# Kernel tuning notes

Hardware: AMD Instinct MI355X
Metric: run time of the kernel (lower is better)

## Reference

```python
import jax, jax.numpy as jnp
import numpy as np

NUM_TAGS = 64
BSZ = 256
SEQ_LEN = 2048


def setup_inputs() -> dict:
    key = jax.random.key(0)
    k1, k2, k3, k4, k5 = jax.random.split(key, 5)
    inputs = jax.random.normal(k1, (BSZ, SEQ_LEN, NUM_TAGS), dtype=jnp.float32)
    tags = jax.random.randint(k2, (BSZ, SEQ_LEN), 0, NUM_TAGS, dtype=jnp.int32)
    mask = jnp.ones((BSZ, SEQ_LEN), dtype=jnp.int32)
    # parameters (xavier-normal-ish transitions, normal start/end)
    std = float(np.sqrt(2.0 / (NUM_TAGS + NUM_TAGS)))
    transitions = jax.random.normal(k3, (NUM_TAGS, NUM_TAGS), dtype=jnp.float32) * std
    start_transitions = jax.random.normal(k4, (NUM_TAGS,), dtype=jnp.float32)
    end_transitions = jax.random.normal(k5, (NUM_TAGS,), dtype=jnp.float32)
    return {"inputs": inputs, "tags": tags, "mask": mask,
            "transitions": transitions,
            "start_transitions": start_transitions,
            "end_transitions": end_transitions}


def _input_likelihood(logits, maskf, transitions, start_transitions, end_transitions):
    # logits: (B, S, T); maskf: (B, S) float
    logits_t = jnp.transpose(logits, (1, 0, 2))   # (S, B, T)
    mask_t = maskf.T                               # (S, B)
    alpha0 = start_transitions[None, :] + logits_t[0]  # (B, T)

    def step(alpha, xs):
        emit, m = xs  # emit: (B, T), m: (B,)
        # inner[b, i, j] = alpha[b, i] + transitions[i, j] + emit[b, j]
        inner = alpha[:, :, None] + transitions[None, :, :] + emit[:, None, :]
        new_alpha = jax.nn.logsumexp(inner, axis=1)  # (B, T)
        alpha = new_alpha * m[:, None] + alpha * (1.0 - m[:, None])
        return alpha, None

    alpha, _ = jax.lax.scan(step, alpha0, (logits_t[1:], mask_t[1:]))
    stops = alpha + end_transitions[None, :]
    return jax.nn.logsumexp(stops, axis=-1)  # (B,)


def _joint_likelihood(logits, tags, mask, maskf, transitions, start_transitions, end_transitions):
    # logits: (B, S, T); tags, mask: (B, S)
    B = logits.shape[0]
    tags = tags * mask  # zero out padded positions
    score = start_transitions[tags[:, 0]]  # (B,)
    # transition scores for t -> t+1, masked by mask[t+1]
    trans = transitions[tags[:, :-1], tags[:, 1:]] * maskf[:, 1:]  # (B, S-1)
    # emission scores for t in [0, S-2], masked by mask[t]
    emit = jnp.take_along_axis(logits[:, :-1, :], tags[:, :-1, None], axis=2)[..., 0]
    emit = emit * maskf[:, :-1]  # (B, S-1)
    score = score + trans.sum(axis=1) + emit.sum(axis=1)
    # last valid tag
    last_idx = maskf.sum(axis=1).astype(jnp.int32) - 1  # (B,)
    batch_ar = jnp.arange(B)
    last_tags = tags[batch_ar, last_idx]  # (B,)
    last_transition_score = end_transitions[last_tags]
    last_input_score = logits[:, -1, :][batch_ar, last_tags]  # (B,)
    score = score + last_transition_score + last_input_score * maskf[:, -1]
    return score  # (B,)


def reference(inputs, tags, mask, transitions, start_transitions, end_transitions):
    maskf = mask.astype(jnp.float32)
    log_denominator = _input_likelihood(inputs, maskf, transitions,
                                        start_transitions, end_transitions)
    log_numerator = _joint_likelihood(inputs, tags, mask, maskf, transitions,
                                      start_transitions, end_transitions)
    return jnp.sum(log_numerator - log_denominator)
```

## Files before the change

### kernel.cpp

```cpp
#include <hip/hip_runtime.h>

#define BSZ 256
#define SEQ 2048
#define NT  64
#define CL  16
#define NC  128
#define SC  256
#define NG  8
#define KS  5.0f

#define SROW  136
#define SSLAB 2184

typedef __fp16 half2_t __attribute__((ext_vector_type(2)));
typedef __fp16 half4_t __attribute__((ext_vector_type(4)));
typedef float  f32x4_t __attribute__((ext_vector_type(4)));
typedef int    int2_t  __attribute__((ext_vector_type(2)));

static __device__ __forceinline__ float wave_red_sum(float x) {
#pragma unroll
    for (int d = 1; d < 64; d <<= 1) x += __shfl_xor(x, d);
    return x;
}

static __device__ __forceinline__ half4_t pack4(float a, float b, float c, float d) {
    half2_t lo = __builtin_amdgcn_cvt_pkrtz(a, b);
    half2_t hi = __builtin_amdgcn_cvt_pkrtz(c, d);
    int2_t t;
    t.x = __builtin_bit_cast(int, lo);
    t.y = __builtin_bit_cast(int, hi);
    return __builtin_bit_cast(half4_t, t);
}

__global__ __launch_bounds__(128) void crf_fat_kernel(
    const float* __restrict__ logits,
    const int*   __restrict__ tags,
    const int*   __restrict__ mask,
    const float* __restrict__ trans,
    const float* __restrict__ startT,
    const float* __restrict__ endT,
    float* __restrict__ rbuf,
    float* __restrict__ wbuf,
    float* __restrict__ Cf,
    float* __restrict__ numtrans)
{
    __shared__ __align__(16) unsigned char Flds[16 * SSLAB];
    __shared__ int lmbits[16];

    if (blockIdx.x < BSZ) {
        const int b   = blockIdx.x;
        const int tid = threadIdx.x;
        __shared__ float redf[128];
        __shared__ int   redi[128];

        const int*   __restrict__ tg = tags + (size_t)b * SEQ;
        const int*   __restrict__ mk = mask + (size_t)b * SEQ;
        const float* __restrict__ Lr = logits + (size_t)b * SEQ * NT;

        float acc = 0.0f;
        int   cnt = 0;
        for (int t = tid; t < SEQ; t += 128) {
            int mt  = mk[t];
            cnt += mt;
            int tgt = tg[t] * mt;
            if (t < SEQ - 1) {
                int m1 = mk[t + 1];
                acc += trans[tgt * NT + tg[t + 1] * m1] * (float)m1;
                acc += Lr[t * NT + tgt] * (float)mt;
            }
        }
        redf[tid] = acc;
        redi[tid] = cnt;
        __syncthreads();
        for (int off = 64; off > 0; off >>= 1) {
            if (tid < off) {
                redf[tid] += redf[tid + off];
                redi[tid] += redi[tid + off];
            }
            __syncthreads();
        }
        if (tid == 0) {
            int   last_idx = redi[0] - 1;
            int   m_last   = mk[SEQ - 1];
            int   tag0     = tg[0] * mk[0];
            int   last_tag = tg[last_idx] * mk[last_idx];
            float r = redf[0] + startT[tag0] + endT[last_tag];
            r += Lr[(size_t)(SEQ - 1) * NT + last_tag] * (float)m_last;
            numtrans[b] = r;
        }
        return;
    }

    const int blk  = blockIdx.x - BSZ;
    const int b    = blk >> 3;
    const int g    = blk & (NG - 1);
    const int tid  = threadIdx.x;
    const bool fwd = (tid >> 6) == 0;
    const int lane = tid & 63;
    const int rlo  = lane & 15;
    const int h    = lane >> 4;

    const float* __restrict__ Lg = logits + ((size_t)b * SEQ + (size_t)g * SC) * NT;
#pragma unroll
    for (int rr = 0; rr < 2; ++rr) {
        int row = tid + rr * 128;
        int s   = row & 15;
        int k   = row >> 4;
        const float* src = Lg + (size_t)row * NT;
        unsigned char* dst = Flds + s * SSLAB + k * SROW;
#pragma unroll
        for (int jj = 0; jj < 16; ++jj) {
            f32x4_t x = *(const f32x4_t*)(src + jj * 4);
            half2_t p0 = __builtin_amdgcn_cvt_pkrtz(__expf(x[0] - KS), __expf(x[1] - KS));
            half2_t p1 = __builtin_amdgcn_cvt_pkrtz(__expf(x[2] - KS), __expf(x[3] - KS));
            int2_t w;
            w.x = __builtin_bit_cast(int, p0);
            w.y = __builtin_bit_cast(int, p1);
            *(int2_t*)(dst + jj * 8) = w;
        }
    }
    if (tid < 16) {
        const int* mk = mask + (size_t)b * SEQ + (size_t)g * SC + tid * CL;
        int bits = 0;
#pragma unroll
        for (int s = 0; s < CL; ++s) bits |= (mk[s] ? 1 : 0) << s;
        if (g == 0 && tid == 0) bits &= ~1;
        lmbits[tid] = bits;
    }

    half4_t A[4][4];
#pragma unroll
    for (int q = 0; q < 4; ++q)
#pragma unroll
        for (int kc = 0; kc < 4; ++kc) {
            float e[4];
#pragma unroll
            for (int i = 0; i < 4; ++i) {
                int m = 16 * q + rlo;
                int k = 16 * kc + 4 * h + i;
                e[i] = __expf(fwd ? trans[k * NT + m] : trans[m * NT + k]);
            }
            A[q][kc] = pack4(e[0], e[1], e[2], e[3]);
        }

    __syncthreads();

    const int mbits = lmbits[rlo];
    f32x4_t V[4];
    float C = 0.0f;
#pragma unroll
    for (int q = 0; q < 4; ++q)
#pragma unroll
        for (int i = 0; i < 4; ++i) V[q][i] = 1.0f;

    if (fwd && g == 0 && rlo == 0) {
        float mx = -1e30f;
        f32x4_t al[4];
#pragma unroll
        for (int q = 0; q < 4; ++q) {
            f32x4_t em = *(const f32x4_t*)(logits + (size_t)b * SEQ * NT + 16 * q + 4 * h);
            f32x4_t st = *(const f32x4_t*)(startT + 16 * q + 4 * h);
#pragma unroll
            for (int i = 0; i < 4; ++i) {
                al[q][i] = st[i] + em[i];
                mx = fmaxf(mx, al[q][i]);
            }
        }
        mx = fmaxf(mx, __shfl_xor(mx, 16));
        mx = fmaxf(mx, __shfl_xor(mx, 32));
        C = mx;
#pragma unroll
        for (int q = 0; q < 4; ++q)
#pragma unroll
            for (int i = 0; i < 4; ++i) V[q][i] = __expf(al[q][i] - mx);
    }

    const unsigned char* Fbase = Flds + rlo * SROW + h * 8;

    auto RENORM = [&](bool track) {
        float mx = V[0][0];
#pragma unroll
        for (int q = 0; q < 4; ++q)
#pragma unroll
            for (int i = 0; i < 4; ++i) mx = fmaxf(mx, V[q][i]);
        mx = fmaxf(mx, __shfl_xor(mx, 16));
        mx = fmaxf(mx, __shfl_xor(mx, 32));
        mx = fmaxf(mx, 1e-30f);
        float inv = 1.0f / mx;
#pragma unroll
        for (int q = 0; q < 4; ++q)
#pragma unroll
            for (int i = 0; i < 4; ++i) V[q][i] *= inv;
        if (track) C += __logf(mx);
    };

    if (fwd) {
#pragma unroll
        for (int s = 0; s < CL; ++s) {
            half4_t Fh[4];
#pragma unroll
            for (int q = 0; q < 4; ++q)
                Fh[q] = *(const half4_t*)(Fbase + s * SSLAB + q * 32);
            half4_t Xh[4];
#pragma unroll
            for (int kc = 0; kc < 4; ++kc)
                Xh[kc] = pack4(V[kc][0], V[kc][1], V[kc][2], V[kc][3]);
            f32x4_t Y[4];
#pragma unroll
            for (int q = 0; q < 4; ++q) {
                f32x4_t acc = {0.0f, 0.0f, 0.0f, 0.0f};
#pragma unroll
                for (int kc = 0; kc < 4; ++kc)
                    acc = __builtin_amdgcn_mfma_f32_16x16x16f16(A[q][kc], Xh[kc], acc, 0, 0, 0);
                Y[q] = acc;
            }
            int mt = (mbits >> s) & 1;
#pragma unroll
            for (int q = 0; q < 4; ++q)
#pragma unroll
                for (int i = 0; i < 4; ++i) {
                    float w = Y[q][i] * (float)Fh[q][i];
                    V[q][i] = mt ? w : V[q][i];
                }
            C += mt ? KS : 0.0f;
            if ((s & 7) == 7) RENORM(true);
        }
        float* op = rbuf + ((size_t)b * NC + g * 16 + rlo) * NT + 4 * h;
#pragma unroll
        for (int q = 0; q < 4; ++q) *(f32x4_t*)(op + 16 * q) = V[q];
        if (h == 0) Cf[b * NC + g * 16 + rlo] = C;
    } else {
#pragma unroll
        for (int s = CL - 1; s >= 0; --s) {
            half4_t Fh[4];
#pragma unroll
            for (int kc = 0; kc < 4; ++kc)
                Fh[kc] = *(const half4_t*)(Fbase + s * SSLAB + kc * 32);
            half4_t Xh[4];
#pragma unroll
            for (int kc = 0; kc < 4; ++kc)
                Xh[kc] = pack4(V[kc][0] * (float)Fh[kc][0],
                               V[kc][1] * (float)Fh[kc][1],
                               V[kc][2] * (float)Fh[kc][2],
                               V[kc][3] * (float)Fh[kc][3]);
            f32x4_t Y[4];
#pragma unroll
            for (int q = 0; q < 4; ++q) {
                f32x4_t acc = {0.0f, 0.0f, 0.0f, 0.0f};
#pragma unroll
                for (int kc = 0; kc < 4; ++kc)
                    acc = __builtin_amdgcn_mfma_f32_16x16x16f16(A[q][kc], Xh[kc], acc, 0, 0, 0);
                Y[q] = acc;
            }
            int mt = (mbits >> s) & 1;
#pragma unroll
            for (int q = 0; q < 4; ++q)
#pragma unroll
                for (int i = 0; i < 4; ++i)
                    V[q][i] = mt ? Y[q][i] : V[q][i];
            if ((s & 7) == 0) RENORM(false);
        }
        float* op = wbuf + ((size_t)b * NC + g * 16 + rlo) * NT + 4 * h;
#pragma unroll
        for (int q = 0; q < 4; ++q) *(f32x4_t*)(op + 16 * q) = V[q];
    }
}

__global__ __launch_bounds__(256) void crf_glue_kernel(
    const float* __restrict__ rbuf,
    const float* __restrict__ wbuf,
    const float* __restrict__ Cf,
    const float* __restrict__ endT,
    float* __restrict__ den_part)
{
    const int batch = blockIdx.x >> 2;
    const int g     = blockIdx.x & 3;
    const int tid   = threadIdx.x;
    const int lane  = tid & 63;
    const int w     = tid >> 6;

    const float* rb = rbuf + (size_t)batch * NC * NT;
    const float* wb = wbuf + (size_t)batch * NC * NT;

    float x = 0.0f;
    if (g == 0) {
        for (int c = tid; c < NC; c += 256) x += Cf[batch * NC + c];
    }

    float part = 0.0f;
    for (int c = 1 + 4 * g + w; c < NC; c += 16) {
        float rprev = rb[(c - 1) * NT + lane];
        float wc    = wb[c * NT + lane];
        float dot = wave_red_sum(rprev * wc);
        float rho = wave_red_sum(wc);
        part += __logf(dot) - __logf(rho);
    }
    if (lane == 0) x += part;
    if (g == 0 && w == 0) {
        float fin = wave_red_sum(rb[(NC - 1) * NT + lane] * __expf(endT[lane]));
        if (lane == 0) x += __logf(fin);
    }

    __shared__ float sred[256];
    sred[tid] = x;
    __syncthreads();
    for (int off = 128; off > 0; off >>= 1) {
        if (tid < off) sred[tid] += sred[tid + off];
        __syncthreads();
    }
    if (tid == 0) den_part[batch * 4 + g] = sred[0];
}

__global__ __launch_bounds__(256) void crf_reduce_kernel(
    const float* __restrict__ den_part,
    const float* __restrict__ numtrans,
    float* __restrict__ out)
{
    __shared__ float red[256];
    const int tid = threadIdx.x;
    float d = den_part[4 * tid] + den_part[4 * tid + 1] +
              den_part[4 * tid + 2] + den_part[4 * tid + 3];
    red[tid] = numtrans[tid] - d;
    __syncthreads();
    for (int off = 128; off > 0; off >>= 1) {
        if (tid < off) red[tid] += red[tid + off];
        __syncthreads();
    }
    if (tid == 0) out[0] = red[0];
}

extern "C" void kernel_launch(void* const* d_in, const int* in_sizes, int n_in,
                              void* d_out, int out_size, void* d_ws, size_t ws_size,
                              hipStream_t stream)
{
    const float* logits = (const float*)d_in[0];
    const int*   tags   = (const int*)  d_in[1];
    const int*   mask   = (const int*)  d_in[2];
    const float* trans  = (const float*)d_in[3];
    const float* startT = (const float*)d_in[4];
    const float* endT   = (const float*)d_in[5];
    float* out = (float*)d_out;
    float* ws  = (float*)d_ws;

    float* den_part = ws;
    float* numtrans = ws + 4 * BSZ;
    float* Cf       = numtrans + BSZ;
    float* rbuf     = Cf + (size_t)BSZ * NC;
    float* wbuf     = rbuf + (size_t)BSZ * NC * NT;

    crf_fat_kernel<<<BSZ + BSZ * NG, 128, 0, stream>>>(
        logits, tags, mask, trans, startT, endT, rbuf, wbuf, Cf, numtrans);
    crf_glue_kernel<<<BSZ * 4, 256, 0, stream>>>(rbuf, wbuf, Cf, endT, den_part);
    crf_reduce_kernel<<<1, 256, 0, stream>>>(den_part, numtrans, out);
}
```

Baseline: 68.99 us.

## Template chunk length and use shorter chunks for more parallel blocks

The scan chunk length becomes a template parameter, and the launcher picks 8-step chunks when the workspace is large enough, falling back to 16 otherwise. Halving the chunk length doubles the number of scan blocks and shortens each block's serial dependency chain, at the cost of twice as many boundary vectors for the glue kernel to write and reduce. The MFMA accumulation is also split into two independent chains to cut dependency latency. The numerator block now reuses the LDS staging buffer for its reductions, and the logits staging loop is reindexed for coalesced loads.

```diff
diff --git a/kernel.cpp b/kernel.cpp
--- a/kernel.cpp
+++ b/kernel.cpp
@@ -3,14 +3,10 @@
 #define BSZ 256
 #define SEQ 2048
 #define NT  64
-#define CL  16
-#define NC  128
-#define SC  256
-#define NG  8
 #define KS  5.0f
 
 #define SROW  136
-#define SSLAB 2184
+#define SSLAB (16 * SROW + 8)
 
 typedef __fp16 half2_t __attribute__((ext_vector_type(2)));
 typedef __fp16 half4_t __attribute__((ext_vector_type(4)));
@@ -32,6 +28,7 @@
     return __builtin_bit_cast(half4_t, t);
 }
 
+template<int CLT>
 __global__ __launch_bounds__(128) void crf_fat_kernel(
     const float* __restrict__ logits,
     const int*   __restrict__ tags,
@@ -44,14 +41,18 @@
     float* __restrict__ Cf,
     float* __restrict__ numtrans)
 {
-    __shared__ __align__(16) unsigned char Flds[16 * SSLAB];
+    constexpr int SCc = 16 * CLT;
+    constexpr int NGc = SEQ / SCc;
+    constexpr int NCc = SEQ / CLT;
+
+    __shared__ __align__(16) unsigned char Flds[CLT * SSLAB];
     __shared__ int lmbits[16];
 
     if (blockIdx.x < BSZ) {
         const int b   = blockIdx.x;
         const int tid = threadIdx.x;
-        __shared__ float redf[128];
-        __shared__ int   redi[128];
+        float* redf = (float*)Flds;
+        int*   redi = (int*)(Flds + 512);
 
         const int*   __restrict__ tg = tags + (size_t)b * SEQ;
         const int*   __restrict__ mk = mask + (size_t)b * SEQ;
@@ -92,38 +93,35 @@
     }
 
     const int blk  = blockIdx.x - BSZ;
-    const int b    = blk >> 3;
-    const int g    = blk & (NG - 1);
+    const int b    = blk / NGc;
+    const int g    = blk % NGc;
     const int tid  = threadIdx.x;
     const bool fwd = (tid >> 6) == 0;
     const int lane = tid & 63;
     const int rlo  = lane & 15;
     const int h    = lane >> 4;
 
-    const float* __restrict__ Lg = logits + ((size_t)b * SEQ + (size_t)g * SC) * NT;
-#pragma unroll
-    for (int rr = 0; rr < 2; ++rr) {
-        int row = tid + rr * 128;
-        int s   = row & 15;
-        int k   = row >> 4;
-        const float* src = Lg + (size_t)row * NT;
-        unsigned char* dst = Flds + s * SSLAB + k * SROW;
-#pragma unroll
-        for (int jj = 0; jj < 16; ++jj) {
-            f32x4_t x = *(const f32x4_t*)(src + jj * 4);
-            half2_t p0 = __builtin_amdgcn_cvt_pkrtz(__expf(x[0] - KS), __expf(x[1] - KS));
-            half2_t p1 = __builtin_amdgcn_cvt_pkrtz(__expf(x[2] - KS), __expf(x[3] - KS));
-            int2_t w;
-            w.x = __builtin_bit_cast(int, p0);
-            w.y = __builtin_bit_cast(int, p1);
-            *(int2_t*)(dst + jj * 8) = w;
-        }
+    const float* __restrict__ Lg = logits + ((size_t)b * SEQ + (size_t)g * SCc) * NT;
+#pragma unroll
+    for (int it = 0; it < 2 * CLT; ++it) {
+        int gci = it * 128 + tid;
+        int row = gci >> 4;
+        int col = gci & 15;
+        int k   = row / CLT;
+        int s   = row % CLT;
+        f32x4_t x = *(const f32x4_t*)(Lg + (size_t)row * NT + col * 4);
+        half2_t p0 = __builtin_amdgcn_cvt_pkrtz(__expf(x[0] - KS), __expf(x[1] - KS));
+        half2_t p1 = __builtin_amdgcn_cvt_pkrtz(__expf(x[2] - KS), __expf(x[3] - KS));
+        int2_t w;
+        w.x = __builtin_bit_cast(int, p0);
+        w.y = __builtin_bit_cast(int, p1);
+        *(int2_t*)(Flds + s * SSLAB + k * SROW + col * 8) = w;
     }
     if (tid < 16) {
-        const int* mk = mask + (size_t)b * SEQ + (size_t)g * SC + tid * CL;
+        const int* mk = mask + (size_t)b * SEQ + (size_t)g * SCc + tid * CLT;
         int bits = 0;
 #pragma unroll
-        for (int s = 0; s < CL; ++s) bits |= (mk[s] ? 1 : 0) << s;
+        for (int s = 0; s < CLT; ++s) bits |= (mk[s] ? 1 : 0) << s;
         if (g == 0 && tid == 0) bits &= ~1;
         lmbits[tid] = bits;
     }
@@ -196,7 +194,7 @@
 
     if (fwd) {
 #pragma unroll
-        for (int s = 0; s < CL; ++s) {
+        for (int s = 0; s < CLT; ++s) {
             half4_t Fh[4];
 #pragma unroll
             for (int q = 0; q < 4; ++q)
@@ -208,11 +206,13 @@
             f32x4_t Y[4];
 #pragma unroll
             for (int q = 0; q < 4; ++q) {
-                f32x4_t acc = {0.0f, 0.0f, 0.0f, 0.0f};
-#pragma unroll
-                for (int kc = 0; kc < 4; ++kc)
-                    acc = __builtin_amdgcn_mfma_f32_16x16x16f16(A[q][kc], Xh[kc], acc, 0, 0, 0);
-                Y[q] = acc;
+                f32x4_t a0 = {0.0f, 0.0f, 0.0f, 0.0f};
+                f32x4_t a1 = {0.0f, 0.0f, 0.0f, 0.0f};
+                a0 = __builtin_amdgcn_mfma_f32_16x16x16f16(A[q][0], Xh[0], a0, 0, 0, 0);
+                a0 = __builtin_amdgcn_mfma_f32_16x16x16f16(A[q][1], Xh[1], a0, 0, 0, 0);
+                a1 = __builtin_amdgcn_mfma_f32_16x16x16f16(A[q][2], Xh[2], a1, 0, 0, 0);
+                a1 = __builtin_amdgcn_mfma_f32_16x16x16f16(A[q][3], Xh[3], a1, 0, 0, 0);
+                Y[q] = a0 + a1;
             }
             int mt = (mbits >> s) & 1;
 #pragma unroll
@@ -225,13 +225,13 @@
             C += mt ? KS : 0.0f;
             if ((s & 7) == 7) RENORM(true);
         }
-        float* op = rbuf + ((size_t)b * NC + g * 16 + rlo) * NT + 4 * h;
+        float* op = rbuf + ((size_t)b * NCc + g * 16 + rlo) * NT + 4 * h;
 #pragma unroll
         for (int q = 0; q < 4; ++q) *(f32x4_t*)(op + 16 * q) = V[q];
-        if (h == 0) Cf[b * NC + g * 16 + rlo] = C;
+        if (h == 0) Cf[b * NCc + g * 16 + rlo] = C;
     } else {
 #pragma unroll
-        for (int s = CL - 1; s >= 0; --s) {
+        for (int s = CLT - 1; s >= 0; --s) {
             half4_t Fh[4];
 #pragma unroll
             for (int kc = 0; kc < 4; ++kc)
@@ -246,11 +246,13 @@
             f32x4_t Y[4];
 #pragma unroll
             for (int q = 0; q < 4; ++q) {
-                f32x4_t acc = {0.0f, 0.0f, 0.0f, 0.0f};
-#pragma unroll
-                for (int kc = 0; kc < 4; ++kc)
-                    acc = __builtin_amdgcn_mfma_f32_16x16x16f16(A[q][kc], Xh[kc], acc, 0, 0, 0);
-                Y[q] = acc;
+                f32x4_t a0 = {0.0f, 0.0f, 0.0f, 0.0f};
+                f32x4_t a1 = {0.0f, 0.0f, 0.0f, 0.0f};
+                a0 = __builtin_amdgcn_mfma_f32_16x16x16f16(A[q][0], Xh[0], a0, 0, 0, 0);
+                a0 = __builtin_amdgcn_mfma_f32_16x16x16f16(A[q][1], Xh[1], a0, 0, 0, 0);
+                a1 = __builtin_amdgcn_mfma_f32_16x16x16f16(A[q][2], Xh[2], a1, 0, 0, 0);
+                a1 = __builtin_amdgcn_mfma_f32_16x16x16f16(A[q][3], Xh[3], a1, 0, 0, 0);
+                Y[q] = a0 + a1;
             }
             int mt = (mbits >> s) & 1;
 #pragma unroll
@@ -260,12 +262,13 @@
                     V[q][i] = mt ? Y[q][i] : V[q][i];
             if ((s & 7) == 0) RENORM(false);
         }
-        float* op = wbuf + ((size_t)b * NC + g * 16 + rlo) * NT + 4 * h;
+        float* op = wbuf + ((size_t)b * NCc + g * 16 + rlo) * NT + 4 * h;
 #pragma unroll
         for (int q = 0; q < 4; ++q) *(f32x4_t*)(op + 16 * q) = V[q];
     }
 }
 
+template<int CLT>
 __global__ __launch_bounds__(256) void crf_glue_kernel(
     const float* __restrict__ rbuf,
     const float* __restrict__ wbuf,
@@ -273,22 +276,23 @@
     const float* __restrict__ endT,
     float* __restrict__ den_part)
 {
+    constexpr int NCc = SEQ / CLT;
     const int batch = blockIdx.x >> 2;
     const int g     = blockIdx.x & 3;
     const int tid   = threadIdx.x;
     const int lane  = tid & 63;
     const int w     = tid >> 6;
 
-    const float* rb = rbuf + (size_t)batch * NC * NT;
-    const float* wb = wbuf + (size_t)batch * NC * NT;
+    const float* rb = rbuf + (size_t)batch * NCc * NT;
+    const float* wb = wbuf + (size_t)batch * NCc * NT;
 
     float x = 0.0f;
     if (g == 0) {
-        for (int c = tid; c < NC; c += 256) x += Cf[batch * NC + c];
+        for (int c = tid; c < NCc; c += 256) x += Cf[batch * NCc + c];
     }
 
     float part = 0.0f;
-    for (int c = 1 + 4 * g + w; c < NC; c += 16) {
+    for (int c = 1 + 4 * g + w; c < NCc; c += 16) {
         float rprev = rb[(c - 1) * NT + lane];
         float wc    = wb[c * NT + lane];
         float dot = wave_red_sum(rprev * wc);
@@ -297,7 +301,7 @@
     }
     if (lane == 0) x += part;
     if (g == 0 && w == 0) {
-        float fin = wave_red_sum(rb[(NC - 1) * NT + lane] * __expf(endT[lane]));
+        float fin = wave_red_sum(rb[(NCc - 1) * NT + lane] * __expf(endT[lane]));
         if (lane == 0) x += __logf(fin);
     }
 
@@ -329,6 +333,32 @@
     if (tid == 0) out[0] = red[0];
 }
 
+template<int CLT>
+static size_t ws_need() {
+    constexpr int NCc = SEQ / CLT;
+    return ((size_t)5 * BSZ + (size_t)BSZ * NCc +
+            2 * (size_t)BSZ * NCc * NT) * sizeof(float);
+}
+
+template<int CLT>
+static void launch_all(const float* logits, const int* tags, const int* mask,
+                       const float* trans, const float* startT, const float* endT,
+                       float* out, float* ws, hipStream_t stream)
+{
+    constexpr int NCc = SEQ / CLT;
+    constexpr int NGc = SEQ / (16 * CLT);
+    float* den_part = ws;
+    float* numtrans = ws + 4 * BSZ;
+    float* Cf       = numtrans + BSZ;
+    float* rbuf     = Cf + (size_t)BSZ * NCc;
+    float* wbuf     = rbuf + (size_t)BSZ * NCc * NT;
+
+    crf_fat_kernel<CLT><<<BSZ + BSZ * NGc, 128, 0, stream>>>(
+        logits, tags, mask, trans, startT, endT, rbuf, wbuf, Cf, numtrans);
+    crf_glue_kernel<CLT><<<BSZ * 4, 256, 0, stream>>>(rbuf, wbuf, Cf, endT, den_part);
+    crf_reduce_kernel<<<1, 256, 0, stream>>>(den_part, numtrans, out);
+}
+
 extern "C" void kernel_launch(void* const* d_in, const int* in_sizes, int n_in,
                               void* d_out, int out_size, void* d_ws, size_t ws_size,
                               hipStream_t stream)
@@ -342,14 +372,9 @@
     float* out = (float*)d_out;
     float* ws  = (float*)d_ws;
 
-    float* den_part = ws;
-    float* numtrans = ws + 4 * BSZ;
-    float* Cf       = numtrans + BSZ;
-    float* rbuf     = Cf + (size_t)BSZ * NC;
-    float* wbuf     = rbuf + (size_t)BSZ * NC * NT;
-
-    crf_fat_kernel<<<BSZ + BSZ * NG, 128, 0, stream>>>(
-        logits, tags, mask, trans, startT, endT, rbuf, wbuf, Cf, numtrans);
-    crf_glue_kernel<<<BSZ * 4, 256, 0, stream>>>(rbuf, wbuf, Cf, endT, den_part);
-    crf_reduce_kernel<<<1, 256, 0, stream>>>(den_part, numtrans, out);
-}
+    if (ws_size >= ws_need<8>()) {
+        launch_all<8>(logits, tags, mask, trans, startT, endT, out, ws, stream);
+    } else {
+        launch_all<16>(logits, tags, mask, trans, startT, endT, out, ws, stream);
+    }
+}
```

Measured after the change: 76.81 us. 11.3% more time.
